# Performance work log

Hardware: AMD Instinct MI355X
Metric: run time of the kernel (lower is better)

Reference implementation:

```python
import jax, jax.numpy as jnp
import numpy as np

B, C, H, W = 128, 2048, 14, 14
K = 112          # num_concepts
NUM_CLASSES = 200


def setup_inputs() -> dict:
    key = jax.random.key(0)
    ks = jax.random.split(key, 8)
    x = jax.random.normal(ks[0], (B, C, H, W), dtype=jnp.float32)
    concepts = jax.random.normal(ks[1], (K, C), dtype=jnp.float32)
    modulation = jax.random.normal(ks[2], (1, C), dtype=jnp.float32)
    background = jax.random.normal(ks[3], (1, C), dtype=jnp.float32)
    # concept_fc: Linear(C, 1)
    w_cfc = jax.random.normal(ks[4], (1, C), dtype=jnp.float32) / np.sqrt(C)
    b_cfc = jnp.zeros((1,), dtype=jnp.float32)
    # label_fc: Linear(C*K, num_classes)
    w_lfc = jax.random.normal(ks[5], (NUM_CLASSES, C * K), dtype=jnp.float32) / np.sqrt(C * K)
    b_lfc = jnp.zeros((NUM_CLASSES,), dtype=jnp.float32)
    return {"x": x, "concepts": concepts, "modulation": modulation,
            "background": background, "w_cfc": w_cfc, "b_cfc": b_cfc,
            "w_lfc": w_lfc, "b_lfc": b_lfc}


def reference(x, concepts, modulation, background, w_cfc, b_cfc, w_lfc, b_lfc):
    b, c, h, w = x.shape
    n = h * w
    x_flat = x.reshape(b, c, n).transpose(0, 2, 1)          # [b, n, c]
    cpts_wbg = jnp.concatenate([concepts, background], 0)   # [k+1, c]

    # cdist p=2 via ||a||^2 + ||x||^2 - 2 a.x
    a_sq = jnp.sum(cpts_wbg * cpts_wbg, -1)                 # [k+1]
    x_sq = jnp.sum(x_flat * x_flat, -1)                     # [b, n]
    dots = jnp.einsum('kc,bnc->bkn', cpts_wbg, x_flat)      # [b, k+1, n]
    d2 = a_sq[None, :, None] + x_sq[:, None, :] - 2.0 * dots
    dists = jnp.sqrt(jnp.maximum(d2, 0.0))                  # [b, k+1, n]

    attn = jax.nn.softmax(-dists, axis=1)                   # softmax over concepts
    cpt_score_maps = attn.reshape(b, -1, h, w)              # [b, k+1, h, w]

    cpt_reprs = jnp.einsum('bkn,bnc->bkc', attn[:, :-1, :], x_flat)  # [b, k, c]
    cpt_logits = jax.nn.sigmoid(
        jnp.einsum('bkc,oc->bko', cpt_reprs, w_cfc) + b_cfc).squeeze(-1)  # [b, k]

    g = cpt_logits[..., None]                               # [b, k, 1]
    cpts_mixed = g * concepts[None] + (1.0 - g) * modulation[None]  # [b, k, c]
    label_logits = cpts_mixed.reshape(b, -1) @ w_lfc.T + b_lfc      # [b, classes]

    return cpt_score_maps, cpt_logits, label_logits
```

## Files before the change

### kernel.cpp

```cpp
#include <hip/hip_runtime.h>
#include <hip/hip_bf16.h>
#include <math.h>

#define B 128
#define C 2048
#define N 196
#define K 112
#define KB 113
#define MROWS 128
#define XWROW 113
#define NCLS 200
#define CKC (C * K)
#define BKP 72
#define NITER 32

#define OUT1_OFF 2834944
#define OUT2_OFF 2849280

typedef __attribute__((ext_vector_type(8))) short bf16x8;
typedef __attribute__((ext_vector_type(4))) float f32x4;

__device__ inline unsigned short f2bf(float f) {
    union { float f; unsigned u; } v; v.f = f;
    unsigned r = v.u + 0x7FFFu + ((v.u >> 16) & 1u);
    return (unsigned short)(r >> 16);
}
__device__ inline unsigned pack2(float a, float b) {
    return (unsigned)f2bf(a) | ((unsigned)f2bf(b) << 16);
}
__device__ inline const float* row_src(int row, const float* concepts,
                                       const float* background, const float* wcfc) {
    if (row < K) return concepts + (size_t)row * C;
    if (row == K) return background;
    if (row == XWROW) return wcfc;
    return nullptr;
}

__global__ __launch_bounds__(256)
void asq_kernel(const float* __restrict__ concepts, const float* __restrict__ background,
                const float* __restrict__ wcfc, float* __restrict__ asq) {
    const int row = blockIdx.x;
    const int tid = threadIdx.x;
    const float* src = row_src(row, concepts, background, wcfc);
    float local = 0.f;
    if (src) for (int i = tid; i < C; i += 256) { float v = src[i]; local += v * v; }
    for (int off = 32; off; off >>= 1) local += __shfl_down(local, off);
    __shared__ float red[4];
    if ((tid & 63) == 0) red[tid >> 6] = local;
    __syncthreads();
    if (tid == 0) asq[row] = red[0] + red[1] + red[2] + red[3];
}

__global__ __launch_bounds__(64)
void pack_kernel(const float* __restrict__ concepts, const float* __restrict__ background,
                 const float* __restrict__ wcfc, unsigned short* __restrict__ Afrag) {
    const int t = blockIdx.x;
    const int kw = blockIdx.y;
    const int l = threadIdx.x;
    const int row = 16 * t + (l & 15);
    const int kb = 32 * kw + 8 * (l >> 4);
    const float* src = row_src(row, concepts, background, wcfc);
    unsigned o[4] = {0u, 0u, 0u, 0u};
    if (src) {
        const float4 f0 = *reinterpret_cast<const float4*>(src + kb);
        const float4 f1 = *reinterpret_cast<const float4*>(src + kb + 4);
        o[0] = pack2(f0.x, f0.y); o[1] = pack2(f0.z, f0.w);
        o[2] = pack2(f1.x, f1.y); o[3] = pack2(f1.z, f1.w);
    }
    *reinterpret_cast<uint4*>(Afrag + (((size_t)t * 64 + kw) * 64 + l) * 8) =
        make_uint4(o[0], o[1], o[2], o[3]);
}

__global__ __launch_bounds__(256)
void main_kernel(const float* __restrict__ x,
                 const unsigned short* __restrict__ Afrag,
                 const float* __restrict__ asq_g,
                 float* __restrict__ out0,
                 float* __restrict__ lpart) {
    __shared__ __align__(16) char smem[38400];
    unsigned short* XT0 = (unsigned short*)smem;
    unsigned short* XT1 = (unsigned short*)(smem + 9216);
    float* dotsL = (float*)smem;
    float* xsqp  = (float*)(smem + 33792);
    float* asq_s = (float*)(smem + 35840);
    float* pm    = (float*)(smem + 36352);
    float* ps    = (float*)(smem + 37376);

    const int tid = threadIdx.x;
    const int lane = tid & 63;
    const int w = tid >> 6;
    const int nt4 = blockIdx.x;
    const int b = blockIdx.y;
    const int n0 = nt4 * 64;

    const int kc = tid >> 5;
    const int pr = tid & 31;
    const int ns = n0 + 2 * pr;
    const bool v0 = ns < N, v1 = (ns + 1) < N;
    const unsigned mA = v0 ? 0xFFFFFFFFu : 0u;
    const unsigned mB = v1 ? 0xFFFFFFFFu : 0u;
    const int nsc = (ns < N - 2) ? ns : (N - 2);
    const float* xcl = x + (size_t)b * C * N + nsc;

    f32x4 acc[2][4];
#pragma unroll
    for (int i = 0; i < 2; ++i)
#pragma unroll
        for (int j = 0; j < 4; ++j) acc[i][j] = (f32x4){0.f, 0.f, 0.f, 0.f};
    float xs0 = 0.f, xs1 = 0.f;

#define STAGE_LOAD(R, it) do {                                                  \
        const float* pb_ = xcl + (size_t)((it) * 64 + kc * 8) * N;              \
        _Pragma("unroll")                                                       \
        for (int e = 0; e < 8; ++e)                                             \
            R[e] = *reinterpret_cast<const float2*>(pb_ + (size_t)e * N);       \
    } while (0)

#define LOAD_A(A, it) do {                                                      \
        _Pragma("unroll")                                                       \
        for (int rt_ = 0; rt_ < 2; ++rt_)                                       \
            _Pragma("unroll")                                                   \
            for (int kw_ = 0; kw_ < 2; ++kw_)                                   \
                A[rt_ * 2 + kw_] = *reinterpret_cast<const bf16x8*>(            \
                    Afrag + ((((size_t)(2 * w + rt_)) * 64 + (it) * 2 + kw_)    \
                             * 64 + lane) * 8);                                 \
    } while (0)

#define PACK_WRITE(R, XTB) do {                                                 \
        unsigned w0_[4], w1_[4];                                                \
        _Pragma("unroll")                                                       \
        for (int q_ = 0; q_ < 4; ++q_) {                                        \
            const float2 ra_ = R[2 * q_], rb_ = R[2 * q_ + 1];                  \
            xs0 += ra_.x * ra_.x + rb_.x * rb_.x;                               \
            xs1 += ra_.y * ra_.y + rb_.y * rb_.y;                               \
            w0_[q_] = pack2(ra_.x, rb_.x) & mA;                                 \
            w1_[q_] = pack2(ra_.y, rb_.y) & mB;                                 \
        }                                                                       \
        *reinterpret_cast<uint4*>(XTB + (size_t)(2 * pr) * BKP + kc * 8) =      \
            make_uint4(w0_[0], w0_[1], w0_[2], w0_[3]);                         \
        *reinterpret_cast<uint4*>(XTB + (size_t)(2 * pr + 1) * BKP + kc * 8) =  \
            make_uint4(w1_[0], w1_[1], w1_[2], w1_[3]);                         \
    } while (0)

#define MFMA_PHASE(A, XTB) do {                                                 \
        _Pragma("unroll")                                                       \
        for (int kw_ = 0; kw_ < 2; ++kw_) {                                     \
            _Pragma("unroll")                                                   \
            for (int nt_ = 0; nt_ < 4; ++nt_) {                                 \
                const bf16x8 bv_ = *reinterpret_cast<const bf16x8*>(            \
                    XTB + (size_t)(nt_ * 16 + (lane & 15)) * BKP                \
                        + kw_ * 32 + (lane >> 4) * 8);                          \
                acc[0][nt_] = __builtin_amdgcn_mfma_f32_16x16x32_bf16(          \
                    A[kw_], bv_, acc[0][nt_], 0, 0, 0);                         \
                acc[1][nt_] = __builtin_amdgcn_mfma_f32_16x16x32_bf16(          \
                    A[2 + kw_], bv_, acc[1][nt_], 0, 0, 0);                     \
            }                                                                   \
        }                                                                       \
    } while (0)

#define BAR() do {                                                              \
        asm volatile("s_waitcnt lgkmcnt(0)" ::: "memory");                      \
        __builtin_amdgcn_s_barrier();                                           \
        __builtin_amdgcn_sched_barrier(0);                                      \
    } while (0)

    float2 rA[8], rB[8];
    bf16x8 aA[4], aB[4];
    STAGE_LOAD(rA, 0);
    STAGE_LOAD(rB, 1);
    LOAD_A(aA, 0);
    LOAD_A(aB, 1);

    for (int itp = 0; itp < 16; ++itp) {
        const int it0 = 2 * itp;
        PACK_WRITE(rA, XT0);
        if (it0 + 2 < NITER) STAGE_LOAD(rA, it0 + 2);
        BAR();
        MFMA_PHASE(aA, XT0);
        if (it0 + 2 < NITER) LOAD_A(aA, it0 + 2);
        PACK_WRITE(rB, XT1);
        if (it0 + 3 < NITER) STAGE_LOAD(rB, it0 + 3);
        BAR();
        MFMA_PHASE(aB, XT1);
        if (it0 + 3 < NITER) LOAD_A(aB, it0 + 3);
    }

    __syncthreads();
#pragma unroll
    for (int rt = 0; rt < 2; ++rt)
#pragma unroll
        for (int nt = 0; nt < 4; ++nt)
#pragma unroll
            for (int rr = 0; rr < 4; ++rr)
                dotsL[(size_t)(16 * (2 * w + rt) + 4 * (lane >> 4) + rr) * 66 +
                      nt * 16 + (lane & 15)] = acc[rt][nt][rr];
    xsqp[kc * 64 + 2 * pr] = xs0;
    xsqp[kc * 64 + 2 * pr + 1] = xs1;
    if (tid < MROWS) asq_s[tid] = asq_g[tid];
    __syncthreads();

    const int j = tid & 63;
    const int q = tid >> 6;
    float xsq = 0.f;
#pragma unroll
    for (int g = 0; g < 8; ++g) xsq += xsqp[g * 64 + j];
    const int rbeg = 29 * q;
    const int rend = (rbeg + 29 < KB) ? rbeg + 29 : KB;

    float m = -3.4e38f;
    for (int row = rbeg; row < rend; ++row) {
        const float d2 = asq_s[row] + xsq - 2.f * dotsL[(size_t)row * 66 + j];
        const float L = -sqrtf(fmaxf(d2, 0.f));
        dotsL[(size_t)row * 66 + j] = L;
        m = fmaxf(m, L);
    }
    pm[q * 64 + j] = m;
    __syncthreads();
    const float M = fmaxf(fmaxf(pm[j], pm[64 + j]), fmaxf(pm[128 + j], pm[192 + j]));
    float s = 0.f;
    for (int row = rbeg; row < rend; ++row) s += __expf(dotsL[(size_t)row * 66 + j] - M);
    ps[q * 64 + j] = s;
    __syncthreads();
    const float S = ps[j] + ps[64 + j] + ps[128 + j] + ps[192 + j];
    const float invS = 1.f / S;
    const float xw = dotsL[(size_t)XWROW * 66 + j];

    const bool jv = (n0 + j) < N;
    float* o0 = out0 + (size_t)b * KB * N + n0 + j;
    for (int row = rbeg; row < rend; ++row) {
        const float a = __expf(dotsL[(size_t)row * 66 + j] - M) * invS;
        if (jv) o0[(size_t)row * N] = a;
        if (row < K) {
            float p = a * xw;
            for (int off = 32; off; off >>= 1) p += __shfl_down(p, off);
            if (j == 0) lpart[((size_t)b * 4 + nt4) * K + row] = p;
        }
    }
}

__global__ __launch_bounds__(256)
void pq_kernel(const float* __restrict__ wlfc, const float* __restrict__ concepts,
               const float* __restrict__ modulation,
               float* __restrict__ Rm, float* __restrict__ Qs) {
    const int wid = (blockIdx.x * 256 + threadIdx.x) >> 6;
    const int lane = threadIdx.x & 63;
    if (wid >= NCLS * K) return;
    const int o = wid / K;
    const int k = wid % K;
    const float4* wp = reinterpret_cast<const float4*>(wlfc + (size_t)o * CKC + (size_t)k * C);
    const float4* cp = reinterpret_cast<const float4*>(concepts + (size_t)k * C);
    const float4* mp = reinterpret_cast<const float4*>(modulation);
    float s1 = 0.f, s2 = 0.f;
#pragma unroll
    for (int it = 0; it < 8; ++it) {
        const int idx = it * 64 + lane;
        const float4 w4 = wp[idx];
        const float4 c4 = cp[idx];
        const float4 m4 = mp[idx];
        s1 += w4.x * c4.x + w4.y * c4.y + w4.z * c4.z + w4.w * c4.w;
        s2 += w4.x * m4.x + w4.y * m4.y + w4.z * m4.z + w4.w * m4.w;
    }
    for (int off = 32; off; off >>= 1) {
        s1 += __shfl_down(s1, off);
        s2 += __shfl_down(s2, off);
    }
    if (lane == 0) { Rm[wid] = s1 - s2; Qs[wid] = s2; }
}

__global__ __launch_bounds__(256)
void final_kernel(const float* __restrict__ lpart, const float* __restrict__ bcfc,
                  const float* __restrict__ Rm, const float* __restrict__ Qs,
                  const float* __restrict__ blfc,
                  float* __restrict__ out1, float* __restrict__ out2) {
    const int b = blockIdx.x;
    const int tid = threadIdx.x;
    __shared__ float g_s[K];
    if (tid < K) {
        const float* lp = lpart + (size_t)b * 4 * K + tid;
        const float v = lp[0] + lp[K] + lp[2 * K] + lp[3 * K] + bcfc[0];
        const float g = 1.f / (1.f + __expf(-v));
        out1[b * K + tid] = g;
        g_s[tid] = g;
    }
    __syncthreads();
    if (tid < NCLS) {
        float acc = blfc[tid];
        const float* rp = Rm + (size_t)tid * K;
        const float* qp = Qs + (size_t)tid * K;
        for (int k = 0; k < K; ++k) acc = fmaf(g_s[k], rp[k], acc) + qp[k];
        out2[b * NCLS + tid] = acc;
    }
}

extern "C" void kernel_launch(void* const* d_in, const int* in_sizes, int n_in,
                              void* d_out, int out_size, void* d_ws, size_t ws_size,
                              hipStream_t stream) {
    const float* x          = (const float*)d_in[0];
    const float* concepts   = (const float*)d_in[1];
    const float* modulation = (const float*)d_in[2];
    const float* background = (const float*)d_in[3];
    const float* wcfc       = (const float*)d_in[4];
    const float* bcfc       = (const float*)d_in[5];
    const float* wlfc       = (const float*)d_in[6];
    const float* blfc       = (const float*)d_in[7];

    float* out  = (float*)d_out;
    float* out0 = out;
    float* out1 = out + OUT1_OFF;
    float* out2 = out + OUT2_OFF;

    float* ws    = (float*)d_ws;
    float* asq   = ws;
    float* lpart = asq + MROWS;
    float* Rm    = lpart + (size_t)B * 4 * K;
    float* Qs    = Rm + NCLS * K;
    unsigned short* Afrag = (unsigned short*)(Qs + NCLS * K);

    asq_kernel<<<MROWS, 256, 0, stream>>>(concepts, background, wcfc, asq);
    pack_kernel<<<dim3(8, 64), 64, 0, stream>>>(concepts, background, wcfc, Afrag);
    main_kernel<<<dim3(4, B), 256, 0, stream>>>(x, Afrag, asq, out0, lpart);
    pq_kernel<<<(NCLS * K) / 4, 256, 0, stream>>>(wlfc, concepts, modulation, Rm, Qs);
    final_kernel<<<B, 256, 0, stream>>>(lpart, bcfc, Rm, Qs, blfc, out1, out2);
}
```

Before: 127.5 us.

## Deepen x prefetch to four register stages and use hardware bf16 packing

```diff
diff --git a/kernel.cpp b/kernel.cpp
--- a/kernel.cpp
+++ b/kernel.cpp
@@ -12,7 +12,7 @@
 #define NCLS 200
 #define CKC (C * K)
 #define BKP 72
-#define NITER 32
+#define XADV (64 * N)
 
 #define OUT1_OFF 2834944
 #define OUT2_OFF 2849280
@@ -20,13 +20,11 @@
 typedef __attribute__((ext_vector_type(8))) short bf16x8;
 typedef __attribute__((ext_vector_type(4))) float f32x4;
 
-__device__ inline unsigned short f2bf(float f) {
-    union { float f; unsigned u; } v; v.f = f;
-    unsigned r = v.u + 0x7FFFu + ((v.u >> 16) & 1u);
-    return (unsigned short)(r >> 16);
-}
-__device__ inline unsigned pack2(float a, float b) {
-    return (unsigned)f2bf(a) | ((unsigned)f2bf(b) << 16);
+__device__ inline unsigned cvtpk(float a, float b) {
+    union { __hip_bfloat162 h; unsigned u; } c;
+    c.h.x = __float2bfloat16(a);
+    c.h.y = __float2bfloat16(b);
+    return c.u;
 }
 __device__ inline const float* row_src(int row, const float* concepts,
                                        const float* background, const float* wcfc) {
@@ -64,14 +62,14 @@
     if (src) {
         const float4 f0 = *reinterpret_cast<const float4*>(src + kb);
         const float4 f1 = *reinterpret_cast<const float4*>(src + kb + 4);
-        o[0] = pack2(f0.x, f0.y); o[1] = pack2(f0.z, f0.w);
-        o[2] = pack2(f1.x, f1.y); o[3] = pack2(f1.z, f1.w);
+        o[0] = cvtpk(f0.x, f0.y); o[1] = cvtpk(f0.z, f0.w);
+        o[2] = cvtpk(f1.x, f1.y); o[3] = cvtpk(f1.z, f1.w);
     }
     *reinterpret_cast<uint4*>(Afrag + (((size_t)t * 64 + kw) * 64 + l) * 8) =
         make_uint4(o[0], o[1], o[2], o[3]);
 }
 
-__global__ __launch_bounds__(256)
+__global__ __launch_bounds__(256, 2)
 void main_kernel(const float* __restrict__ x,
                  const unsigned short* __restrict__ Afrag,
                  const float* __restrict__ asq_g,
@@ -100,7 +98,7 @@
     const unsigned mA = v0 ? 0xFFFFFFFFu : 0u;
     const unsigned mB = v1 ? 0xFFFFFFFFu : 0u;
     const int nsc = (ns < N - 2) ? ns : (N - 2);
-    const float* xcl = x + (size_t)b * C * N + nsc;
+    const float* xstage = x + (size_t)b * C * N + nsc + (size_t)kc * 8 * N;
 
     f32x4 acc[2][4];
 #pragma unroll
@@ -109,11 +107,16 @@
         for (int j = 0; j < 4; ++j) acc[i][j] = (f32x4){0.f, 0.f, 0.f, 0.f};
     float xs0 = 0.f, xs1 = 0.f;
 
-#define STAGE_LOAD(R, it) do {                                                  \
-        const float* pb_ = xcl + (size_t)((it) * 64 + kc * 8) * N;              \
-        _Pragma("unroll")                                                       \
-        for (int e = 0; e < 8; ++e)                                             \
-            R[e] = *reinterpret_cast<const float2*>(pb_ + (size_t)e * N);       \
+#define STAGE_LOAD(R) do {                                                      \
+        (R##0) = *reinterpret_cast<const float2*>(xstage + (size_t)0 * N);      \
+        (R##1) = *reinterpret_cast<const float2*>(xstage + (size_t)1 * N);      \
+        (R##2) = *reinterpret_cast<const float2*>(xstage + (size_t)2 * N);      \
+        (R##3) = *reinterpret_cast<const float2*>(xstage + (size_t)3 * N);      \
+        (R##4) = *reinterpret_cast<const float2*>(xstage + (size_t)4 * N);      \
+        (R##5) = *reinterpret_cast<const float2*>(xstage + (size_t)5 * N);      \
+        (R##6) = *reinterpret_cast<const float2*>(xstage + (size_t)6 * N);      \
+        (R##7) = *reinterpret_cast<const float2*>(xstage + (size_t)7 * N);      \
+        xstage += XADV;                                                         \
     } while (0)
 
 #define LOAD_A(A, it) do {                                                      \
@@ -128,14 +131,22 @@
 
 #define PACK_WRITE(R, XTB) do {                                                 \
         unsigned w0_[4], w1_[4];                                                \
-        _Pragma("unroll")                                                       \
-        for (int q_ = 0; q_ < 4; ++q_) {                                        \
-            const float2 ra_ = R[2 * q_], rb_ = R[2 * q_ + 1];                  \
-            xs0 += ra_.x * ra_.x + rb_.x * rb_.x;                               \
-            xs1 += ra_.y * ra_.y + rb_.y * rb_.y;                               \
-            w0_[q_] = pack2(ra_.x, rb_.x) & mA;                                 \
-            w1_[q_] = pack2(ra_.y, rb_.y) & mB;                                 \
-        }                                                                       \
+        xs0 += (R##0).x * (R##0).x + (R##1).x * (R##1).x;                       \
+        xs1 += (R##0).y * (R##0).y + (R##1).y * (R##1).y;                       \
+        w0_[0] = cvtpk((R##0).x, (R##1).x) & mA;                                \
+        w1_[0] = cvtpk((R##0).y, (R##1).y) & mB;                                \
+        xs0 += (R##2).x * (R##2).x + (R##3).x * (R##3).x;                       \
+        xs1 += (R##2).y * (R##2).y + (R##3).y * (R##3).y;                       \
+        w0_[1] = cvtpk((R##2).x, (R##3).x) & mA;                                \
+        w1_[1] = cvtpk((R##2).y, (R##3).y) & mB;                                \
+        xs0 += (R##4).x * (R##4).x + (R##5).x * (R##5).x;                       \
+        xs1 += (R##4).y * (R##4).y + (R##5).y * (R##5).y;                       \
+        w0_[2] = cvtpk((R##4).x, (R##5).x) & mA;                                \
+        w1_[2] = cvtpk((R##4).y, (R##5).y) & mB;                                \
+        xs0 += (R##6).x * (R##6).x + (R##7).x * (R##7).x;                       \
+        xs1 += (R##6).y * (R##6).y + (R##7).y * (R##7).y;                       \
+        w0_[3] = cvtpk((R##6).x, (R##7).x) & mA;                                \
+        w1_[3] = cvtpk((R##6).y, (R##7).y) & mB;                                \
         *reinterpret_cast<uint4*>(XTB + (size_t)(2 * pr) * BKP + kc * 8) =      \
             make_uint4(w0_[0], w0_[1], w0_[2], w0_[3]);                         \
         *reinterpret_cast<uint4*>(XTB + (size_t)(2 * pr + 1) * BKP + kc * 8) =  \
@@ -164,26 +175,30 @@
         __builtin_amdgcn_sched_barrier(0);                                      \
     } while (0)
 
-    float2 rA[8], rB[8];
+    float2 rA0, rA1, rA2, rA3, rA4, rA5, rA6, rA7;
+    float2 rB0, rB1, rB2, rB3, rB4, rB5, rB6, rB7;
+    float2 rC0, rC1, rC2, rC3, rC4, rC5, rC6, rC7;
+    float2 rD0, rD1, rD2, rD3, rD4, rD5, rD6, rD7;
     bf16x8 aA[4], aB[4];
-    STAGE_LOAD(rA, 0);
-    STAGE_LOAD(rB, 1);
-    LOAD_A(aA, 0);
-    LOAD_A(aB, 1);
-
-    for (int itp = 0; itp < 16; ++itp) {
-        const int it0 = 2 * itp;
-        PACK_WRITE(rA, XT0);
-        if (it0 + 2 < NITER) STAGE_LOAD(rA, it0 + 2);
-        BAR();
-        MFMA_PHASE(aA, XT0);
-        if (it0 + 2 < NITER) LOAD_A(aA, it0 + 2);
-        PACK_WRITE(rB, XT1);
-        if (it0 + 3 < NITER) STAGE_LOAD(rB, it0 + 3);
-        BAR();
-        MFMA_PHASE(aB, XT1);
-        if (it0 + 3 < NITER) LOAD_A(aB, it0 + 3);
-    }
+
+    STAGE_LOAD(rA); STAGE_LOAD(rB); STAGE_LOAD(rC); STAGE_LOAD(rD);
+    LOAD_A(aA, 0); LOAD_A(aB, 1);
+
+    for (int itp = 0; itp < 7; ++itp) {
+        const int j0 = 4 * itp;
+        PACK_WRITE(rA, XT0); STAGE_LOAD(rA); BAR();
+        MFMA_PHASE(aA, XT0); LOAD_A(aA, j0 + 2);
+        PACK_WRITE(rB, XT1); STAGE_LOAD(rB); BAR();
+        MFMA_PHASE(aB, XT1); LOAD_A(aB, j0 + 3);
+        PACK_WRITE(rC, XT0); STAGE_LOAD(rC); BAR();
+        MFMA_PHASE(aA, XT0); LOAD_A(aA, j0 + 4);
+        PACK_WRITE(rD, XT1); STAGE_LOAD(rD); BAR();
+        MFMA_PHASE(aB, XT1); LOAD_A(aB, j0 + 5);
+    }
+    PACK_WRITE(rA, XT0); BAR(); MFMA_PHASE(aA, XT0); LOAD_A(aA, 30);
+    PACK_WRITE(rB, XT1); BAR(); MFMA_PHASE(aB, XT1); LOAD_A(aB, 31);
+    PACK_WRITE(rC, XT0); BAR(); MFMA_PHASE(aA, XT0);
+    PACK_WRITE(rD, XT1); BAR(); MFMA_PHASE(aB, XT1);
 
     __syncthreads();
 #pragma unroll
```

After: 128.0 us. Within noise of the previous version (+0.4%).
